# Kernel optimization log

Hardware: AMD Instinct MI355X
Metric: run time of the kernel (lower is better)

## Reference

```python
import jax, jax.numpy as jnp
import numpy as np

B, T, C = 16, 64, 512


def setup_inputs() -> dict:
    key = jax.random.key(0)
    ks = jax.random.split(key, 12)
    s = 1.0 / np.sqrt(C)
    st = 1.0 / np.sqrt(2.0)
    return {
        "x": jax.random.normal(ks[0], (B, T, C), dtype=jnp.float32),
        "ts": jax.random.uniform(ks[1], (B, T), dtype=jnp.float32),
        "attn_mask": jnp.ones((B, T), dtype=jnp.float32),
        # project: Linear(C, C)
        "W_proj": jax.random.uniform(ks[2], (C, C), jnp.float32, -s, s),
        "b_proj": jax.random.uniform(ks[3], (C,), jnp.float32, -s, s),
        # embed_xs: Linear(C, C)
        "W_x": jax.random.uniform(ks[4], (C, C), jnp.float32, -s, s),
        "b_x": jax.random.uniform(ks[5], (C,), jnp.float32, -s, s),
        # embed_ts: Linear(2, C)
        "W_t": jax.random.uniform(ks[6], (2, C), jnp.float32, -st, st),
        "b_t": jax.random.uniform(ks[7], (C,), jnp.float32, -st, st),
        # get_importances Linear(C, C)
        "W_imp": jax.random.uniform(ks[8], (C, C), jnp.float32, -s, s),
        "b_imp": jax.random.uniform(ks[9], (C,), jnp.float32, -s, s),
    }


def reference(x, ts, attn_mask, W_proj, b_proj, W_x, b_x, W_t, b_t, W_imp, b_imp):
    # x: [B,T,C], ts: [B,T], attn_mask: [B,T]
    values = (x @ W_proj + b_proj)[:, None, :, :]          # [B,1,T,C]
    rel = ts[:, :, None] - ts[:, None, :]                  # [B,T,T]
    rel2 = jnp.log1p(jnp.maximum(jnp.stack([rel, -rel], axis=-1), 0.0))  # [B,T,T,2]
    h = rel2 @ W_t + b_t                                   # [B,T,T,C] (include_t)
    h = h + (x @ W_x + b_x)[:, None, :, :]                 # include_x, broadcast over dim 1
    importances = jax.nn.sigmoid(jax.nn.relu(h) @ W_imp + b_imp)  # [B,T,T,C]
    importances = importances * attn_mask[:, None, :, None]
    interactions = jax.nn.logsumexp(values * importances, axis=2)  # [B,T,C]
    return (x + interactions, importances.mean(axis=3))
```

## Files before the change

kernel.cpp:

```cpp
#include <hip/hip_runtime.h>
#include <hip/hip_bf16.h>

#define Bn 16
#define Tn 64
#define Cn 512
#define LDA  520
#define LDA8 528

#define LOG2E 1.4426950408889634f
#define LN2   0.6931471805599453f
#define ASC 16.0f
#define WSC 256.0f
#define ZSC (1.0f/4096.0f)
#define NZL (-(LOG2E)*(ZSC))

typedef short s8v __attribute__((ext_vector_type(8)));
typedef float f4v __attribute__((ext_vector_type(4)));
typedef unsigned long ul2 __attribute__((ext_vector_type(2)));

__device__ __forceinline__ unsigned int pk2bf(float a, float b){
  __hip_bfloat162 t = __float22bfloat162_rn(make_float2(a, b));
  union { __hip_bfloat162 h; unsigned int u; } c; c.h = t; return c.u;
}
__device__ __forceinline__ float bits2f(unsigned int u){
  union { unsigned int u; float f; } c; c.u = u; return c.f;
}
__device__ __forceinline__ s8v pack_bf8(const float* v){
  union { uint4 u; s8v s; } c;
  c.u.x = pk2bf(v[0], v[1]); c.u.y = pk2bf(v[2], v[3]);
  c.u.z = pk2bf(v[4], v[5]); c.u.w = pk2bf(v[6], v[7]);
  return c.s;
}

__global__ __launch_bounds__(256)
void pre(const float* __restrict__ x, const float* __restrict__ ts,
         const float* __restrict__ Wp, const float* __restrict__ bp,
         const float* __restrict__ Wx, const float* __restrict__ bx,
         const float* __restrict__ bt, const float* __restrict__ Wi,
         float* __restrict__ xe, unsigned short* __restrict__ vfrag,
         unsigned char* __restrict__ Wsw8, float* __restrict__ R){
  __shared__ unsigned short lA[Tn * LDA];
  const int blk = blockIdx.x;
  const int tid = threadIdx.x;
  if(blk < 64){
    int gid2 = blk * 256 + tid;
    float r[8];
#pragma unroll
    for(int q = 0; q < 4; ++q){
      int p = gid2 * 4 + q;
      int b = p >> 12, i = (p >> 6) & 63, j = p & 63;
      float d = ts[b * Tn + i] - ts[b * Tn + j];
      r[2*q]   = __logf(1.f + fmaxf(d, 0.f));
      r[2*q+1] = __logf(1.f + fmaxf(-d, 0.f));
    }
    float4* Rf4 = reinterpret_cast<float4*>(R);
    Rf4[gid2 * 2    ] = make_float4(r[0], r[1], r[2], r[3]);
    Rf4[gid2 * 2 + 1] = make_float4(r[4], r[5], r[6], r[7]);
    return;
  }
  if(blk < 192){
    int rem = (blk - 64) * 256 + tid;
    int nt = rem & 3, lane = (rem >> 2) & 63, w8 = (rem >> 8) & 7, s = rem >> 11;
    int n  = (w8 * 4 + nt) * 16 + (lane & 15);
    int k0 = s * 32 + ((lane >> 4) << 3);
    float v[8];
#pragma unroll
    for(int j = 0; j < 8; ++j) v[j] = Wi[(k0 + j) * Cn + n] * WSC;
    int d0 = __builtin_amdgcn_cvt_pk_fp8_f32(v[0], v[1], 0, false);
    d0     = __builtin_amdgcn_cvt_pk_fp8_f32(v[2], v[3], d0, true);
    int d1 = __builtin_amdgcn_cvt_pk_fp8_f32(v[4], v[5], 0, false);
    d1     = __builtin_amdgcn_cvt_pk_fp8_f32(v[6], v[7], d1, true);
    uint2 o; o.x = (unsigned int)d0; o.y = (unsigned int)d1;
    *reinterpret_cast<uint2*>(Wsw8 + (size_t)((s * 8 + w8) * 64 + lane) * 32 + nt * 8) = o;
    return;
  }
  const int idx = blk - 192;
  const int b = idx >> 4, mat = (idx >> 3) & 1, oct = idx & 7;
  const int lane = tid & 63, w2 = tid >> 6, quad = lane >> 4, ln = lane & 15;
  const int t = oct * 4 + w2;
  const float* Wg = mat ? Wx : Wp;
  const float* wb = Wg + (size_t)(quad * 8) * Cn + t * 16 + ln;

  const int c0 = (tid & 127) * 4, jb = tid >> 7;
#pragma unroll
  for(int it = 0; it < 32; ++it){
    int j = jb + it * 2;
    f4v xv = *reinterpret_cast<const f4v*>(x + ((b * Tn + j) * Cn + c0));
    uint2 uu; uu.x = pk2bf(xv[0], xv[1]); uu.y = pk2bf(xv[2], xv[3]);
    *reinterpret_cast<uint2*>(&lA[j * LDA + c0]) = uu;
  }
  float wv[8];
#pragma unroll
  for(int j = 0; j < 8; ++j) wv[j] = wb[j * Cn];
  __syncthreads();

  s8v a[4], an[4];
#pragma unroll
  for(int mt = 0; mt < 4; ++mt)
    a[mt] = *reinterpret_cast<const s8v*>(&lA[(mt * 16 + ln) * LDA + quad * 8]);
  f4v acc[4];
#pragma unroll
  for(int mt = 0; mt < 4; ++mt){ acc[mt][0]=0.f; acc[mt][1]=0.f; acc[mt][2]=0.f; acc[mt][3]=0.f; }
  s8v bcur = pack_bf8(wv);

#pragma unroll 2
  for(int s = 0; s < 16; ++s){
    int sn = (s + 1) & 15;
    float wn[8];
#pragma unroll
    for(int j = 0; j < 8; ++j) wn[j] = wb[(size_t)sn * 32 * Cn + j * Cn];
#pragma unroll
    for(int mt = 0; mt < 4; ++mt)
      an[mt] = *reinterpret_cast<const s8v*>(&lA[(mt * 16 + ln) * LDA + sn * 32 + quad * 8]);
#pragma unroll
    for(int mt = 0; mt < 4; ++mt)
      acc[mt] = __builtin_amdgcn_mfma_f32_16x16x32_bf16(a[mt], bcur, acc[mt], 0, 0, 0);
#pragma unroll
    for(int mt = 0; mt < 4; ++mt) a[mt] = an[mt];
    bcur = pack_bf8(wn);
  }

  const int c = t * 16 + ln;
  if(mat == 0){
    float bb = bp[c];
    const int eb_h = w2 & 1;
#pragma unroll
    for(int mt = 0; mt < 4; ++mt){
      float v0 = (acc[mt][0] + bb) * LOG2E;
      float v1 = (acc[mt][1] + bb) * LOG2E;
      float v2 = (acc[mt][2] + bb) * LOG2E;
      float v3 = (acc[mt][3] + bb) * LOG2E;
      uint2 o; o.x = pk2bf(v0, v1); o.y = pk2bf(v2, v3);
      int eb = mt * 2 + (w2 >> 1);
      *reinterpret_cast<uint2*>(vfrag + ((size_t)((b * 8 + oct) * 8 + eb) * 64 + lane) * 8 + eb_h * 4) = o;
    }
  } else {
    float bb = bx[c] + bt[c];
#pragma unroll
    for(int mt = 0; mt < 4; ++mt)
#pragma unroll
      for(int r = 0; r < 4; ++r){
        int j = mt * 16 + quad * 4 + r;
        xe[(b * Tn + j) * Cn + c] = (acc[mt][r] + bb) * ASC;
      }
  }
}

__global__ __launch_bounds__(512, 4)
void fused(const float* __restrict__ x, const float* __restrict__ am,
           const float* __restrict__ Wt, const float* __restrict__ bimp,
           const unsigned char* __restrict__ Wsw8, const float* __restrict__ R,
           const float* __restrict__ xe, const unsigned short* __restrict__ vfrag,
           float* __restrict__ out0, float* __restrict__ out1){
  __shared__ unsigned char lA8[Tn * LDA8];
  __shared__ float msk[Tn], rr0[Tn], rr1[Tn], rsum[Tn];
  const int b = blockIdx.x >> 6, i = blockIdx.x & 63;
  const int tid = threadIdx.x;
  const int lane = tid & 63, w = tid >> 6, quad = lane >> 4, ln = lane & 15;
  const int ph = (blockIdx.x & 1) << 3;

  float mv = 0.f; float2 rv = make_float2(0.f, 0.f);
  if(tid < Tn){
    mv = am[b * Tn + tid];
    rv = reinterpret_cast<const float2*>(R)[(b * Tn + i) * Tn + tid];
  }

  const int c0 = (tid & 127) * 4, jb = tid >> 7;
  f4v xv[16];
#pragma unroll
  for(int it = 0; it < 16; ++it)
    xv[it] = *reinterpret_cast<const f4v*>(xe + ((b * Tn + (jb + it * 4)) * Cn + c0));

  const ul2* Bv = reinterpret_cast<const ul2*>(Wsw8);
  const int off = (w * 64 + lane) * 2;
  ul2 bA[2], bB[2];
  bA[0] = Bv[ph * 1024 + off];       bB[0] = Bv[ph * 1024 + off + 1];
  bA[1] = Bv[(ph + 1) * 1024 + off]; bB[1] = Bv[(ph + 1) * 1024 + off + 1];

  if(tid < Tn){ msk[tid] = mv; rr0[tid] = rv.x; rr1[tid] = rv.y; rsum[tid] = 0.f; }
  __syncthreads();

  f4v wt0 = *reinterpret_cast<const f4v*>(Wt + c0);
  f4v wt1 = *reinterpret_cast<const f4v*>(Wt + Cn + c0);
  wt0[0]*=ASC; wt0[1]*=ASC; wt0[2]*=ASC; wt0[3]*=ASC;
  wt1[0]*=ASC; wt1[1]*=ASC; wt1[2]*=ASC; wt1[3]*=ASC;
#pragma unroll
  for(int it = 0; it < 16; ++it){
    int j = jb + it * 4;
    float r0 = rr0[j], r1 = rr1[j];
    float h0 = fmaxf(fmaf(r1, wt1[0], fmaf(r0, wt0[0], xv[it][0])), 0.f);
    float h1 = fmaxf(fmaf(r1, wt1[1], fmaf(r0, wt0[1], xv[it][1])), 0.f);
    float h2 = fmaxf(fmaf(r1, wt1[2], fmaf(r0, wt0[2], xv[it][2])), 0.f);
    float h3 = fmaxf(fmaf(r1, wt1[3], fmaf(r0, wt0[3], xv[it][3])), 0.f);
    int d = __builtin_amdgcn_cvt_pk_fp8_f32(h0, h1, 0, false);
    d     = __builtin_amdgcn_cvt_pk_fp8_f32(h2, h3, d, true);
    *reinterpret_cast<int*>(lA8 + j * LDA8 + c0) = d;
  }
  __syncthreads();

  unsigned long a[4], an[4];
#pragma unroll
  for(int mt = 0; mt < 4; ++mt)
    a[mt] = *reinterpret_cast<const unsigned long*>(lA8 + (mt * 16 + ln) * LDA8 + ph * 32 + quad * 8);
  f4v acc[4][4];
#pragma unroll
  for(int mt = 0; mt < 4; ++mt)
#pragma unroll
    for(int nt = 0; nt < 4; ++nt){
      acc[mt][nt][0]=0.f; acc[mt][nt][1]=0.f; acc[mt][nt][2]=0.f; acc[mt][nt][3]=0.f;
    }

#pragma unroll 4
  for(int s = 0; s < 16; ++s){
    const int sc = s & 1;
    const int p2 = (s + 2 + ph) & 15;
    const int p1 = (s + 1 + ph) & 15;
    ul2 nb0 = Bv[p2 * 1024 + off];
    ul2 nb1 = Bv[p2 * 1024 + off + 1];
#pragma unroll
    for(int mt = 0; mt < 4; ++mt)
      an[mt] = *reinterpret_cast<const unsigned long*>(lA8 + (mt * 16 + ln) * LDA8 + p1 * 32 + quad * 8);
    long bf0 = (long)bA[sc].x, bf1 = (long)bA[sc].y;
    long bf2 = (long)bB[sc].x, bf3 = (long)bB[sc].y;
#pragma unroll
    for(int mt = 0; mt < 4; ++mt){
      acc[mt][0] = __builtin_amdgcn_mfma_f32_16x16x32_fp8_fp8((long)a[mt], bf0, acc[mt][0], 0, 0, 0);
      acc[mt][1] = __builtin_amdgcn_mfma_f32_16x16x32_fp8_fp8((long)a[mt], bf1, acc[mt][1], 0, 0, 0);
      acc[mt][2] = __builtin_amdgcn_mfma_f32_16x16x32_fp8_fp8((long)a[mt], bf2, acc[mt][2], 0, 0, 0);
      acc[mt][3] = __builtin_amdgcn_mfma_f32_16x16x32_fp8_fp8((long)a[mt], bf3, acc[mt][3], 0, 0, 0);
    }
#pragma unroll
    for(int mt = 0; mt < 4; ++mt) a[mt] = an[mt];
    bA[sc] = nb0; bB[sc] = nb1;
  }

  uint4 vv[8];
#pragma unroll
  for(int eb = 0; eb < 8; ++eb)
    vv[eb] = *reinterpret_cast<const uint4*>(vfrag + ((size_t)((b * 8 + w) * 8 + eb) * 64 + lane) * 8);
  float xq[4];
#pragma unroll
  for(int nt = 0; nt < 4; ++nt)
    xq[nt] = x[(b * Tn + i) * Cn + (w * 64 + nt * 16 + ln)];

  const unsigned int* vw = reinterpret_cast<const unsigned int*>(vv);
  float bbf[4];
#pragma unroll
  for(int nt = 0; nt < 4; ++nt) bbf[nt] = bimp[w * 64 + nt * 16 + ln] * -LOG2E;
  float se[4] = {0.f, 0.f, 0.f, 0.f};
#pragma unroll
  for(int mt = 0; mt < 4; ++mt)
#pragma unroll
    for(int r = 0; r < 4; ++r){
      float mk = msk[mt * 16 + quad * 4 + r];
      float p = 0.f;
#pragma unroll
      for(int nt = 0; nt < 4; ++nt){
        float zn = fmaf(acc[mt][nt][r], NZL, bbf[nt]);
        float im = mk * __builtin_amdgcn_rcpf(1.f + __builtin_amdgcn_exp2f(zn));
        p += im;
        int e = mt * 16 + nt * 4 + r;
        unsigned int d = vw[e >> 1];
        float vl = bits2f((e & 1) ? (d & 0xffff0000u) : (d << 16));
        se[nt] += __builtin_amdgcn_exp2f(vl * im);
      }
      p += __shfl_xor(p, 1, 64);
      p += __shfl_xor(p, 2, 64);
      p += __shfl_xor(p, 4, 64);
      p += __shfl_xor(p, 8, 64);
      if(ln == 0) atomicAdd(&rsum[mt * 16 + quad * 4 + r], p);
    }
  __syncthreads();
  if(tid < Tn) out1[(b * Tn + i) * Tn + tid] = rsum[tid] * (1.f / 512.f);

#pragma unroll
  for(int nt = 0; nt < 4; ++nt){
    float s0 = se[nt];
    s0 += __shfl_xor(s0, 16, 64);
    s0 += __shfl_xor(s0, 32, 64);
    if(quad == 0){
      int idx = (b * Tn + i) * Cn + (w * 64 + nt * 16 + ln);
      out0[idx] = xq[nt] + __builtin_amdgcn_logf(s0) * LN2;
    }
  }
}

extern "C" void kernel_launch(void* const* d_in, const int* in_sizes, int n_in,
                              void* d_out, int out_size, void* d_ws, size_t ws_size,
                              hipStream_t stream){
  const float* x    = (const float*)d_in[0];
  const float* ts   = (const float*)d_in[1];
  const float* am   = (const float*)d_in[2];
  const float* Wp   = (const float*)d_in[3];
  const float* bp   = (const float*)d_in[4];
  const float* Wx   = (const float*)d_in[5];
  const float* bx   = (const float*)d_in[6];
  const float* Wt   = (const float*)d_in[7];
  const float* bt   = (const float*)d_in[8];
  const float* Wi   = (const float*)d_in[9];
  const float* bimp = (const float*)d_in[10];
  float* out0 = (float*)d_out;
  float* out1 = out0 + Bn * Tn * Cn;

  char* ws = (char*)d_ws;
  unsigned char*  Wsw8  = (unsigned char*)ws;
  float*          xe    = (float*)(ws + 262144);
  unsigned short* vfrag = (unsigned short*)(ws + 2359296);
  float*          R     = (float*)(ws + 3407872);

  pre<<<448, 256, 0, stream>>>(x, ts, Wp, bp, Wx, bx, bt, Wi, xe, vfrag, Wsw8, R);
  fused<<<1024, 512, 0, stream>>>(x, am, Wt, bimp, Wsw8, R, xe, vfrag, out0, out1);
}
```

Baseline: 124.9 us.

## Switch importance GEMM to scaled 16x16x128 FP8 MFMA with repacked weights

Replaces the 16x16x32 FP8 MFMA loop with the MI355X scaled 16x16x128 f8f6f4 MFMA using unit scales. This cuts the number of MFMA instructions and loop iterations by a factor of four. The weight pre-swizzle kernel is rewritten to emit 32-byte K-slices per lane, and the A operand is now read from LDS as two 16-byte loads per tile. The stagger over K steps becomes a 4-way rotation, and the B operand is prefetched one K-step ahead. The trade-offs are higher register pressure from the 8-int fragments and a different LDS access pattern.

Result: slower. 349.2 us (+179.7%).

```diff
diff --git a/kernel.cpp b/kernel.cpp
--- a/kernel.cpp
+++ b/kernel.cpp
@@ -13,10 +13,11 @@
 #define WSC 256.0f
 #define ZSC (1.0f/4096.0f)
 #define NZL (-(LOG2E)*(ZSC))
+#define SC1 0x7F7F7F7FU
 
 typedef short s8v __attribute__((ext_vector_type(8)));
 typedef float f4v __attribute__((ext_vector_type(4)));
-typedef unsigned long ul2 __attribute__((ext_vector_type(2)));
+typedef int   i8v __attribute__((ext_vector_type(8)));
 
 __device__ __forceinline__ unsigned int pk2bf(float a, float b){
   __hip_bfloat162 t = __float22bfloat162_rn(make_float2(a, b));
@@ -31,6 +32,7 @@
   c.u.z = pk2bf(v[4], v[5]); c.u.w = pk2bf(v[6], v[7]);
   return c.s;
 }
+union U8 { uint4 q[2]; i8v v; };
 
 __global__ __launch_bounds__(256)
 void pre(const float* __restrict__ x, const float* __restrict__ ts,
@@ -58,23 +60,30 @@
     Rf4[gid2 * 2 + 1] = make_float4(r[4], r[5], r[6], r[7]);
     return;
   }
-  if(blk < 192){
+  if(blk < 128){
     int rem = (blk - 64) * 256 + tid;
-    int nt = rem & 3, lane = (rem >> 2) & 63, w8 = (rem >> 8) & 7, s = rem >> 11;
-    int n  = (w8 * 4 + nt) * 16 + (lane & 15);
-    int k0 = s * 32 + ((lane >> 4) << 3);
-    float v[8];
-#pragma unroll
-    for(int j = 0; j < 8; ++j) v[j] = Wi[(k0 + j) * Cn + n] * WSC;
-    int d0 = __builtin_amdgcn_cvt_pk_fp8_f32(v[0], v[1], 0, false);
-    d0     = __builtin_amdgcn_cvt_pk_fp8_f32(v[2], v[3], d0, true);
-    int d1 = __builtin_amdgcn_cvt_pk_fp8_f32(v[4], v[5], 0, false);
-    d1     = __builtin_amdgcn_cvt_pk_fp8_f32(v[6], v[7], d1, true);
-    uint2 o; o.x = (unsigned int)d0; o.y = (unsigned int)d1;
-    *reinterpret_cast<uint2*>(Wsw8 + (size_t)((s * 8 + w8) * 64 + lane) * 32 + nt * 8) = o;
+    int p    = rem & 1;
+    int lane = (rem >> 1) & 63;
+    int t    = (rem >> 7) & 31;
+    int s128 = rem >> 12;
+    int quad = lane >> 4, ln = lane & 15;
+    int k0 = s128 * 128 + quad * 32 + p * 16;
+    int n  = t * 16 + ln;
+    float v[16];
+#pragma unroll
+    for(int j = 0; j < 16; ++j) v[j] = Wi[(k0 + j) * Cn + n] * WSC;
+    unsigned int d[4];
+#pragma unroll
+    for(int g = 0; g < 4; ++g){
+      int dd = __builtin_amdgcn_cvt_pk_fp8_f32(v[4*g],   v[4*g+1], 0, false);
+      dd     = __builtin_amdgcn_cvt_pk_fp8_f32(v[4*g+2], v[4*g+3], dd, true);
+      d[g] = (unsigned int)dd;
+    }
+    uint4 o; o.x = d[0]; o.y = d[1]; o.z = d[2]; o.w = d[3];
+    *reinterpret_cast<uint4*>(Wsw8 + (size_t)(s128 * 32 + t) * 2048 + p * 1024 + lane * 16) = o;
     return;
   }
-  const int idx = blk - 192;
+  const int idx = blk - 128;
   const int b = idx >> 4, mat = (idx >> 3) & 1, oct = idx & 7;
   const int lane = tid & 63, w2 = tid >> 6, quad = lane >> 4, ln = lane & 15;
   const int t = oct * 4 + w2;
@@ -157,7 +166,7 @@
   const int b = blockIdx.x >> 6, i = blockIdx.x & 63;
   const int tid = threadIdx.x;
   const int lane = tid & 63, w = tid >> 6, quad = lane >> 4, ln = lane & 15;
-  const int ph = (blockIdx.x & 1) << 3;
+  const int st = blockIdx.x & 3;
 
   float mv = 0.f; float2 rv = make_float2(0.f, 0.f);
   if(tid < Tn){
@@ -171,11 +180,13 @@
   for(int it = 0; it < 16; ++it)
     xv[it] = *reinterpret_cast<const f4v*>(xe + ((b * Tn + (jb + it * 4)) * Cn + c0));
 
-  const ul2* Bv = reinterpret_cast<const ul2*>(Wsw8);
-  const int off = (w * 64 + lane) * 2;
-  ul2 bA[2], bB[2];
-  bA[0] = Bv[ph * 1024 + off];       bB[0] = Bv[ph * 1024 + off + 1];
-  bA[1] = Bv[(ph + 1) * 1024 + off]; bB[1] = Bv[(ph + 1) * 1024 + off + 1];
+  U8 ub[4];
+#pragma unroll
+  for(int nt = 0; nt < 4; ++nt){
+    size_t F = (size_t)(st * 32 + w * 4 + nt) * 2048 + lane * 16;
+    ub[nt].q[0] = *reinterpret_cast<const uint4*>(Wsw8 + F);
+    ub[nt].q[1] = *reinterpret_cast<const uint4*>(Wsw8 + F + 1024);
+  }
 
   if(tid < Tn){ msk[tid] = mv; rr0[tid] = rv.x; rr1[tid] = rv.y; rsum[tid] = 0.f; }
   __syncthreads();
@@ -198,10 +209,6 @@
   }
   __syncthreads();
 
-  unsigned long a[4], an[4];
-#pragma unroll
-  for(int mt = 0; mt < 4; ++mt)
-    a[mt] = *reinterpret_cast<const unsigned long*>(lA8 + (mt * 16 + ln) * LDA8 + ph * 32 + quad * 8);
   f4v acc[4][4];
 #pragma unroll
   for(int mt = 0; mt < 4; ++mt)
@@ -210,28 +217,30 @@
       acc[mt][nt][0]=0.f; acc[mt][nt][1]=0.f; acc[mt][nt][2]=0.f; acc[mt][nt][3]=0.f;
     }
 
-#pragma unroll 4
-  for(int s = 0; s < 16; ++s){
-    const int sc = s & 1;
-    const int p2 = (s + 2 + ph) & 15;
-    const int p1 = (s + 1 + ph) & 15;
-    ul2 nb0 = Bv[p2 * 1024 + off];
-    ul2 nb1 = Bv[p2 * 1024 + off + 1];
-#pragma unroll
-    for(int mt = 0; mt < 4; ++mt)
-      an[mt] = *reinterpret_cast<const unsigned long*>(lA8 + (mt * 16 + ln) * LDA8 + p1 * 32 + quad * 8);
-    long bf0 = (long)bA[sc].x, bf1 = (long)bA[sc].y;
-    long bf2 = (long)bB[sc].x, bf3 = (long)bB[sc].y;
+#pragma unroll
+  for(int sI = 0; sI < 4; ++sI){
+    const int s128 = (st + sI) & 3;
+    i8v bv0 = ub[0].v, bv1 = ub[1].v, bv2 = ub[2].v, bv3 = ub[3].v;
+    if(sI < 3){
+      const int sn = (st + sI + 1) & 3;
+#pragma unroll
+      for(int nt = 0; nt < 4; ++nt){
+        size_t F = (size_t)(sn * 32 + w * 4 + nt) * 2048 + lane * 16;
+        ub[nt].q[0] = *reinterpret_cast<const uint4*>(Wsw8 + F);
+        ub[nt].q[1] = *reinterpret_cast<const uint4*>(Wsw8 + F + 1024);
+      }
+    }
 #pragma unroll
     for(int mt = 0; mt < 4; ++mt){
-      acc[mt][0] = __builtin_amdgcn_mfma_f32_16x16x32_fp8_fp8((long)a[mt], bf0, acc[mt][0], 0, 0, 0);
-      acc[mt][1] = __builtin_amdgcn_mfma_f32_16x16x32_fp8_fp8((long)a[mt], bf1, acc[mt][1], 0, 0, 0);
-      acc[mt][2] = __builtin_amdgcn_mfma_f32_16x16x32_fp8_fp8((long)a[mt], bf2, acc[mt][2], 0, 0, 0);
-      acc[mt][3] = __builtin_amdgcn_mfma_f32_16x16x32_fp8_fp8((long)a[mt], bf3, acc[mt][3], 0, 0, 0);
-    }
-#pragma unroll
-    for(int mt = 0; mt < 4; ++mt) a[mt] = an[mt];
-    bA[sc] = nb0; bB[sc] = nb1;
+      U8 ua;
+      const unsigned char* ap = lA8 + (mt * 16 + ln) * LDA8 + s128 * 128 + quad * 32;
+      ua.q[0] = *reinterpret_cast<const uint4*>(ap);
+      ua.q[1] = *reinterpret_cast<const uint4*>(ap + 16);
+      acc[mt][0] = __builtin_amdgcn_mfma_scale_f32_16x16x128_f8f6f4(ua.v, bv0, acc[mt][0], 0, 0, 0, SC1, 0, SC1);
+      acc[mt][1] = __builtin_amdgcn_mfma_scale_f32_16x16x128_f8f6f4(ua.v, bv1, acc[mt][1], 0, 0, 0, SC1, 0, SC1);
+      acc[mt][2] = __builtin_amdgcn_mfma_scale_f32_16x16x128_f8f6f4(ua.v, bv2, acc[mt][2], 0, 0, 0, SC1, 0, SC1);
+      acc[mt][3] = __builtin_amdgcn_mfma_scale_f32_16x16x128_f8f6f4(ua.v, bv3, acc[mt][3], 0, 0, 0, SC1, 0, SC1);
+    }
   }
 
   uint4 vv[8];
@@ -308,6 +317,6 @@
   unsigned short* vfrag = (unsigned short*)(ws + 2359296);
   float*          R     = (float*)(ws + 3407872);
 
-  pre<<<448, 256, 0, stream>>>(x, ts, Wp, bp, Wx, bx, bt, Wi, xe, vfrag, Wsw8, R);
+  pre<<<384, 256, 0, stream>>>(x, ts, Wp, bp, Wx, bx, bt, Wi, xe, vfrag, Wsw8, R);
   fused<<<1024, 512, 0, stream>>>(x, am, Wt, bimp, Wsw8, R, xe, vfrag, out0, out1);
 }
```
